# Performance work log

Measured on AMD Instinct MI355X. Metric: run time of the kernel, lower is better.

Reference implementation:

```python
import jax, jax.numpy as jnp
import numpy as np

EMBED_DIM = 256


def setup_inputs() -> dict:
    key = jax.random.key(0)
    k1, k2, k3 = jax.random.split(key, 3)
    B, S, E = 4, 256, EMBED_DIM
    component_repr = jax.random.normal(k1, (B, S, E), dtype=jnp.float32)
    # nn.Linear(2E, E): weight [E, 2E], bias [E]
    bound = 1.0 / np.sqrt(2 * E)
    W = jax.random.uniform(k2, (E, 2 * E), minval=-bound, maxval=bound, dtype=jnp.float32)
    b = jax.random.uniform(k3, (E,), minval=-bound, maxval=bound, dtype=jnp.float32)
    return {"component_repr": component_repr, "W": W, "b": b}


def reference(component_repr, W, b):
    # Faithful to: cat([comp_i, comp_j], -1) @ W.T + b
    # Split W into halves acting on comp_i and comp_j; avoids the [B,S,S,2E] concat.
    E = component_repr.shape[-1]
    W1, W2 = W[:, :E], W[:, E:]
    pi = jnp.einsum('bse,fe->bsf', component_repr, W1)  # [B,S,E]
    pj = jnp.einsum('bse,fe->bsf', component_repr, W2)  # [B,S,E]
    # broadcast to pairwise [B,S,S,E]
    return pi[:, :, None, :] + pj[:, None, :, :] + b
```

## Files before the change

kernel.cpp:

```cpp
#include <hip/hip_runtime.h>

typedef __attribute__((ext_vector_type(4))) float float4v;

__global__ __launch_bounds__(256) void transposeW(
    const float* __restrict__ W, float* __restrict__ Wt) {
    __shared__ float tile[64][65];
    const int ta = blockIdx.x & 3;
    const int tc = blockIdx.x >> 2;
    const int lx = threadIdx.x & 63;
    const int ly = threadIdx.x >> 6;
#pragma unroll
    for (int rr = 0; rr < 64; rr += 4)
        tile[rr + ly][lx] = W[(size_t)(ta * 64 + rr + ly) * 512 + tc * 64 + lx];
    __syncthreads();
#pragma unroll
    for (int rr = 0; rr < 64; rr += 4)
        Wt[(size_t)(tc * 64 + rr + ly) * 256 + ta * 64 + lx] = tile[lx][rr + ly];
}

__global__ __launch_bounds__(256) void gemm_pipj(
    const float* __restrict__ x, const float* __restrict__ Wt,
    const float* __restrict__ bias,
    float* __restrict__ pib, float* __restrict__ pj) {
    const int r0 = blockIdx.x * 4;
    const int t = threadIdx.x;
    const int rw = t >> 6;
    const int fq = t & 63;
    __shared__ float xs[4][256];
#pragma unroll
    for (int k = 0; k < 4; ++k)
        ((float*)xs)[k * 256 + t] = x[(size_t)r0 * 256 + k * 256 + t];
    __syncthreads();

    const float4v* wt = (const float4v*)Wt;
    float4v acc0 = {0.f, 0.f, 0.f, 0.f};
    float4v acc1 = {0.f, 0.f, 0.f, 0.f};
#pragma unroll 4
    for (int e = 0; e < 256; ++e) {
        float xv = xs[rw][e];
        float4v w1 = wt[(size_t)e * 64 + fq];
        float4v w2 = wt[(size_t)(e + 256) * 64 + fq];
        acc0 += w1 * xv;
        acc1 += w2 * xv;
    }
    const float4v bv = *(const float4v*)(bias + fq * 4);
    *(float4v*)(pib + (size_t)(r0 + rw) * 256 + fq * 4) = acc0 + bv;
    *(float4v*)(pj  + (size_t)(r0 + rw) * 256 + fq * 4) = acc1;
}

__global__ __launch_bounds__(256) void bcast_add(
    const float* __restrict__ pib, const float* __restrict__ pj,
    float* __restrict__ out) {
    const int bi   = blockIdx.x >> 1;
    const int half = blockIdx.x & 1;
    const int t = threadIdx.x;
    const int w = t >> 6;
    const int f0 = (t & 63) * 4;
    const int b = bi >> 8;
    const int j0 = half * 128 + w * 32;

    const float4v a = *(const float4v*)(pib + (size_t)bi * 256 + f0);
    const float* pjbase = pj + ((size_t)(b * 256 + j0)) * 256 + f0;
    float* obase = out + (((size_t)bi * 256) + j0) * 256 + f0;
#pragma unroll 8
    for (int jj = 0; jj < 32; ++jj) {
        float4v p = *(const float4v*)(pjbase + (size_t)jj * 256);
        *(float4v*)(obase + (size_t)jj * 256) = a + p;
    }
}

extern "C" void kernel_launch(void* const* d_in, const int* in_sizes, int n_in,
                              void* d_out, int out_size, void* d_ws, size_t ws_size,
                              hipStream_t stream) {
    const float* x    = (const float*)d_in[0];
    const float* W    = (const float*)d_in[1];
    const float* bias = (const float*)d_in[2];
    float* out = (float*)d_out;

    float* pib = (float*)d_ws;
    float* pj  = pib + 1024 * 256;
    float* Wt  = pj  + 1024 * 256;

    transposeW<<<32, 256, 0, stream>>>(W, Wt);
    gemm_pipj<<<256, 256, 0, stream>>>(x, Wt, bias, pib, pj);
    bcast_add<<<2048, 256, 0, stream>>>(pib, pj, out);
}
```

Measured before the change: 280.2 us.

## Split K across waves in gemm and reuse W loads for four rows

Each wave in the gemm block now handles a quarter of the reduction dimension for all four rows instead of the full reduction for one row. Each W load is therefore reused four times, and block-wide W traffic from cache drops by four. Partial sums are combined through a shared-memory reduction, which adds an extra barrier, extra LDS, and more accumulator registers.

```diff
diff --git a/kernel.cpp b/kernel.cpp
--- a/kernel.cpp
+++ b/kernel.cpp
@@ -27,25 +27,40 @@
     const int rw = t >> 6;
     const int fq = t & 63;
     __shared__ float xs[4][256];
+    __shared__ float4v red[4][4][2][64];
 #pragma unroll
     for (int k = 0; k < 4; ++k)
         ((float*)xs)[k * 256 + t] = x[(size_t)r0 * 256 + k * 256 + t];
     __syncthreads();
 
     const float4v* wt = (const float4v*)Wt;
-    float4v acc0 = {0.f, 0.f, 0.f, 0.f};
-    float4v acc1 = {0.f, 0.f, 0.f, 0.f};
+    float4v acc0[4] = {{0,0,0,0},{0,0,0,0},{0,0,0,0},{0,0,0,0}};
+    float4v acc1[4] = {{0,0,0,0},{0,0,0,0},{0,0,0,0},{0,0,0,0}};
 #pragma unroll 4
-    for (int e = 0; e < 256; ++e) {
-        float xv = xs[rw][e];
+    for (int ee = 0; ee < 64; ++ee) {
+        const int e = rw * 64 + ee;
         float4v w1 = wt[(size_t)e * 64 + fq];
         float4v w2 = wt[(size_t)(e + 256) * 64 + fq];
-        acc0 += w1 * xv;
-        acc1 += w2 * xv;
+#pragma unroll
+        for (int r = 0; r < 4; ++r) {
+            float xv = xs[r][e];
+            acc0[r] += w1 * xv;
+            acc1[r] += w2 * xv;
+        }
     }
+#pragma unroll
+    for (int r = 0; r < 4; ++r) {
+        red[rw][r][0][fq] = acc0[r];
+        red[rw][r][1][fq] = acc1[r];
+    }
+    __syncthreads();
+    float4v s0 = red[0][rw][0][fq] + red[1][rw][0][fq]
+               + red[2][rw][0][fq] + red[3][rw][0][fq];
+    float4v s1 = red[0][rw][1][fq] + red[1][rw][1][fq]
+               + red[2][rw][1][fq] + red[3][rw][1][fq];
     const float4v bv = *(const float4v*)(bias + fq * 4);
-    *(float4v*)(pib + (size_t)(r0 + rw) * 256 + fq * 4) = acc0 + bv;
-    *(float4v*)(pj  + (size_t)(r0 + rw) * 256 + fq * 4) = acc1;
+    *(float4v*)(pib + (size_t)(r0 + rw) * 256 + fq * 4) = s0 + bv;
+    *(float4v*)(pj  + (size_t)(r0 + rw) * 256 + fq * 4) = s1;
 }
 
 __global__ __launch_bounds__(256) void bcast_add(
```

Result: faster. 265.9 us (-5.1%).
